# Performance work log

Hardware: AMD Instinct MI355X
Metric: run time of the kernel (lower is better)

The kernel has to match this reference:

```python
import jax, jax.numpy as jnp
import numpy as np

N = 100000      # nodes (dtype==2 subgraph)
E = 1600000     # edges
IN_DIM = 256
OUT_DIM = 64
FEAT_DIM = 64   # hard-coded by nn.Linear(64, out_dim) in dstfeat_fc


def setup_inputs() -> dict:
    key = jax.random.key(0)
    k1, k2, k3, k4, k5, k6 = jax.random.split(key, 6)
    h = jax.random.normal(k1, (N, IN_DIM), dtype=jnp.float32)
    feat = jax.random.normal(k2, (N, FEAT_DIM), dtype=jnp.float32)
    W_fc = jax.random.normal(k3, (OUT_DIM, IN_DIM), dtype=jnp.float32) * 0.05
    W_dst = jax.random.normal(k4, (OUT_DIM, FEAT_DIM), dtype=jnp.float32) * 0.05
    src = jax.random.randint(k5, (E,), 0, N, dtype=jnp.int64)
    dst = jax.random.randint(k6, (E,), 0, N, dtype=jnp.int64)
    return {"h": h, "feat": feat, "W_fc": W_fc, "W_dst": W_dst, "src": src, "dst": dst}


def reference(h, feat, W_fc, W_dst, src, dst):
    # node projections (done once per node, then gathered per edge)
    z = h @ W_fc.T            # [N, OUT]  (self.fc)
    df = feat @ W_dst.T       # [N, OUT]  (self.dstfeat_fc on dst 'feat')

    # per-edge attention logit: dot(z[src], dstfeat[dst])
    e = jnp.sum(z[src] * df[dst], axis=-1)          # [E]

    # segment softmax over incoming edges of each destination node
    emax = jax.ops.segment_max(e, dst, num_segments=N)
    emax = jnp.where(jnp.isfinite(emax), emax, 0.0)  # guard empty segments
    ex = jnp.exp(e - emax[dst])                      # [E]
    denom = jax.ops.segment_sum(ex, dst, num_segments=N)  # [N]

    # weighted neighbor aggregation: sum_e alpha_e * z[src_e] per dst
    num = jax.ops.segment_sum(ex[:, None] * z[src], dst, num_segments=N)  # [N, OUT]
    out = num / jnp.where(denom == 0, 1.0, denom)[:, None]
    return out
```

## Files before the change

### kernel.cpp

```cpp
#include <hip/hip_runtime.h>
#include <math.h>

typedef unsigned int uint32;
typedef __attribute__((ext_vector_type(8))) short bf16x8;
typedef __attribute__((ext_vector_type(4))) float f32x4;

__device__ __forceinline__ ushort f2bf(float f) {
  uint32 u = __builtin_bit_cast(uint32, f);
  uint32 r = (u + 0x7fff + ((u >> 16) & 1)) >> 16;
  return (ushort)r;
}
__device__ __forceinline__ float bf_lo(uint32 u) {
  return __builtin_bit_cast(float, u << 16);
}
__device__ __forceinline__ float bf_hi(uint32 u) {
  return __builtin_bit_cast(float, u & 0xffff0000u);
}

template <int K, bool BF16OUT>
__device__ __forceinline__ void gemm_body(const float* __restrict__ A,
                                          const float* __restrict__ W,
                                          ushort* __restrict__ Cb,
                                          float* __restrict__ C,
                                          int M, int bx, ushort* Ws) {
  const int t = threadIdx.x;
  const int lane = t & 63;
  const int w = t >> 6;
  const int quad = lane >> 4;
  const int l16 = lane & 15;
  const int rBase = bx * 128;
  const int WSTR = K + 8;

  const int kq4 = K >> 2;
  for (int idx = t; idx < 64 * kq4; idx += 256) {
    int row = idx / kq4, kq = idx - row * kq4;
    float4 v = *(const float4*)(W + (size_t)row * K + kq * 4);
    ushort4 b;
    b.x = f2bf(v.x); b.y = f2bf(v.y); b.z = f2bf(v.z); b.w = f2bf(v.w);
    *(ushort4*)&Ws[row * WSTR + kq * 4] = b;
  }
  __syncthreads();

  f32x4 acc[2][4];
  #pragma unroll
  for (int i = 0; i < 2; ++i)
    #pragma unroll
    for (int n = 0; n < 4; ++n) acc[i][n] = (f32x4){0.f, 0.f, 0.f, 0.f};

  const int r0 = min(rBase + w * 32 + l16, M - 1);
  const int r1 = min(rBase + w * 32 + 16 + l16, M - 1);
  const float* __restrict__ a0 = A + (size_t)r0 * K + quad * 8;
  const float* __restrict__ a1 = A + (size_t)r1 * K + quad * 8;

  #pragma unroll 2
  for (int kb = 0; kb < K; kb += 32) {
    float4 v00 = *(const float4*)(a0 + kb);
    float4 v01 = *(const float4*)(a0 + kb + 4);
    float4 v10 = *(const float4*)(a1 + kb);
    float4 v11 = *(const float4*)(a1 + kb + 4);
    bf16x8 af0, af1;
    af0[0] = (short)f2bf(v00.x); af0[1] = (short)f2bf(v00.y);
    af0[2] = (short)f2bf(v00.z); af0[3] = (short)f2bf(v00.w);
    af0[4] = (short)f2bf(v01.x); af0[5] = (short)f2bf(v01.y);
    af0[6] = (short)f2bf(v01.z); af0[7] = (short)f2bf(v01.w);
    af1[0] = (short)f2bf(v10.x); af1[1] = (short)f2bf(v10.y);
    af1[2] = (short)f2bf(v10.z); af1[3] = (short)f2bf(v10.w);
    af1[4] = (short)f2bf(v11.x); af1[5] = (short)f2bf(v11.y);
    af1[6] = (short)f2bf(v11.z); af1[7] = (short)f2bf(v11.w);

    bf16x8 bfrag[4];
    #pragma unroll
    for (int n = 0; n < 4; ++n)
      bfrag[n] = *(const bf16x8*)&Ws[(n * 16 + l16) * WSTR + kb + quad * 8];

    #pragma unroll
    for (int n = 0; n < 4; ++n) {
      acc[0][n] = __builtin_amdgcn_mfma_f32_16x16x32_bf16(af0, bfrag[n], acc[0][n], 0, 0, 0);
      acc[1][n] = __builtin_amdgcn_mfma_f32_16x16x32_bf16(af1, bfrag[n], acc[1][n], 0, 0, 0);
    }
  }

  #pragma unroll
  for (int i = 0; i < 2; ++i)
    #pragma unroll
    for (int nt = 0; nt < 4; ++nt)
      #pragma unroll
      for (int r = 0; r < 4; ++r) {
        int row = rBase + w * 32 + i * 16 + quad * 4 + r;
        int col = nt * 16 + l16;
        if (row < M) {
          if (BF16OUT)
            Cb[(size_t)row * 64 + col] = f2bf(acc[i][nt][r]);
          else
            C[(size_t)row * 64 + col] = acc[i][nt][r];
        }
      }
}

__global__ __launch_bounds__(256, 4) void gemm_both(const float* __restrict__ h,
                                                    const float* __restrict__ feat,
                                                    const float* __restrict__ W_fc,
                                                    const float* __restrict__ W_dst,
                                                    ushort* __restrict__ zb,
                                                    float* __restrict__ df,
                                                    int M, int gsplit) {
  __shared__ __align__(16) ushort Ws[64 * 264];
  if ((int)blockIdx.x < gsplit)
    gemm_body<256, true>(h, W_fc, zb, nullptr, M, (int)blockIdx.x, Ws);
  else
    gemm_body<64, false>(feat, W_dst, nullptr, df, M, (int)blockIdx.x - gsplit, Ws);
}

#define NBBITS 8
#define BKNODES 256
#define CH 4096
#define NBMAX 512

__global__ __launch_bounds__(256) void csr_count(const int* __restrict__ dst,
                                                 int* __restrict__ bCnt, int E, int NB) {
  __shared__ int lcnt[NBMAX];
  const int t = threadIdx.x;
  for (int i = t; i < NB; i += 256) lcnt[i] = 0;
  __syncthreads();
  const int c0 = blockIdx.x * CH, c1 = min(c0 + CH, E);
  for (int i = c0 + t; i < c1; i += 256) atomicAdd(&lcnt[dst[i] >> NBBITS], 1);
  __syncthreads();
  for (int b = t; b < NB; b += 256) {
    int c = lcnt[b];
    if (c) atomicAdd(&bCnt[b], c);
  }
}

__global__ __launch_bounds__(512) void csr_scan(const int* __restrict__ bCnt,
                                                int* __restrict__ bBase,
                                                int* __restrict__ bCursor,
                                                int* __restrict__ offsets,
                                                int NB, int N, int E) {
  __shared__ int wsum[8];
  const int t = threadIdx.x;
  const int lane = t & 63, wave = t >> 6;
  int x = (t < NB) ? bCnt[t] : 0;
  int inc = x;
  #pragma unroll
  for (int d = 1; d < 64; d <<= 1) {
    int o = __shfl_up(inc, d, 64);
    if (lane >= d) inc += o;
  }
  if (lane == 63) wsum[wave] = inc;
  __syncthreads();
  int wbase = 0;
  #pragma unroll
  for (int w = 0; w < 8; ++w)
    if (w < wave) wbase += wsum[w];
  int excl = wbase + inc - x;
  if (t < NB) {
    bBase[t] = excl;
    bCursor[t] = excl;
  }
  if (t == 0) {
    bBase[NB] = E;
    offsets[N] = E;
  }
}

__global__ __launch_bounds__(256) void csr_partition(const int* __restrict__ src,
                                                     const int* __restrict__ dst,
                                                     int* __restrict__ bCursor,
                                                     unsigned* __restrict__ packed,
                                                     int E, int NB) {
  __shared__ int lcnt[NBMAX];
  __shared__ int lbase[NBMAX];
  const int t = threadIdx.x;
  for (int i = t; i < NB; i += 256) lcnt[i] = 0;
  __syncthreads();
  const int c0 = blockIdx.x * CH, c1 = min(c0 + CH, E);
  for (int i = c0 + t; i < c1; i += 256) atomicAdd(&lcnt[dst[i] >> NBBITS], 1);
  __syncthreads();
  for (int b = t; b < NB; b += 256) {
    int c = lcnt[b];
    lbase[b] = c ? atomicAdd(&bCursor[b], c) : 0;
  }
  __syncthreads();
  for (int i = c0 + t; i < c1; i += 256) {
    int dv = dst[i];
    int b = dv >> NBBITS;
    int pos = atomicAdd(&lbase[b], 1);
    packed[pos] = ((unsigned)src[i] << NBBITS) | (unsigned)(dv & (BKNODES - 1));
  }
}

__global__ __launch_bounds__(256) void csr_finalize(const int* __restrict__ bBase,
                                                    const unsigned* __restrict__ packed,
                                                    int* __restrict__ edgeSrc,
                                                    int* __restrict__ offsets, int N) {
  __shared__ int sh[BKNODES];
  __shared__ int wsum[4];
  const int r = blockIdx.x;
  const int t = threadIdx.x;
  const int lane = t & 63, wave = t >> 6;
  const int base = bBase[r];
  const int endr = bBase[r + 1];
  sh[t] = 0;
  __syncthreads();
  for (int i = base + t; i < endr; i += 256)
    atomicAdd(&sh[packed[i] & (BKNODES - 1)], 1);
  __syncthreads();
  {
    int x = sh[t];
    int inc = x;
    #pragma unroll
    for (int d = 1; d < 64; d <<= 1) {
      int o = __shfl_up(inc, d, 64);
      if (lane >= d) inc += o;
    }
    if (lane == 63) wsum[wave] = inc;
    __syncthreads();
    int wbase = 0;
    #pragma unroll
    for (int w = 0; w < 4; ++w)
      if (w < wave) wbase += wsum[w];
    int excl = wbase + inc - x;
    __syncthreads();
    sh[t] = base + excl;
  }
  __syncthreads();
  const int node0 = r << NBBITS;
  {
    int g = node0 + t;
    if (g < N) offsets[g] = sh[t];
  }
  __syncthreads();
  for (int i = base + t; i < endr; i += 256) {
    unsigned v = packed[i];
    int pos = atomicAdd(&sh[v & (BKNODES - 1)], 1);
    edgeSrc[pos] = (int)(v >> NBBITS);
  }
}

__global__ __launch_bounds__(256) void aggregate(const ushort* __restrict__ zb,
                                                 const float* __restrict__ df,
                                                 const int* __restrict__ offsets,
                                                 const int* __restrict__ edgeSrc,
                                                 float* __restrict__ out, int N, int NW) {
  const int lane = threadIdx.x & 63;
  int d = __builtin_amdgcn_readfirstlane((int)((blockIdx.x * blockDim.x + threadIdx.x) >> 6));
  if (d >= N) return;
  const int g = lane >> 4;
  const int l16 = lane & 15;

  int beg = offsets[d];
  int end = offsets[d + 1];
  float4 df4 = *(const float4*)(df + (size_t)d * 64 + l16 * 4);

  while (true) {
    const int nd = d + NW;
    const int ndc = min(nd, N - 1);
    const int nbeg = offsets[ndc];
    const int nend = offsets[ndc + 1];
    const float4 ndf4 = *(const float4*)(df + (size_t)ndc * 64 + l16 * 4);

    float m = -INFINITY, l = 0.f;
    float ax = 0.f, ay = 0.f, az = 0.f, aw = 0.f;

    for (int j0 = beg; j0 < end; j0 += 32) {
      const int nst = min(8, (end - j0 + 3) >> 2);
      uint2 zf[8];
      float ew[8];
      float bm = -INFINITY;

      #pragma unroll
      for (int st = 0; st < 8; ++st) {
        if (st < nst) {
          const int eidx = j0 + st * 4 + g;
          const bool act = eidx < end;
          int s = 0;
          if (act) s = edgeSrc[eidx];
          zf[st] = *(const uint2*)(zb + (size_t)s * 64 + l16 * 4);
          float p = bf_lo(zf[st].x) * df4.x;
          p = fmaf(bf_hi(zf[st].x), df4.y, p);
          p = fmaf(bf_lo(zf[st].y), df4.z, p);
          p = fmaf(bf_hi(zf[st].y), df4.w, p);
          p += __shfl_xor(p, 1, 64);
          p += __shfl_xor(p, 2, 64);
          p += __shfl_xor(p, 4, 64);
          p += __shfl_xor(p, 8, 64);
          ew[st] = act ? p : -INFINITY;
          bm = fmaxf(bm, ew[st]);
        }
      }
      bm = fmaxf(bm, __shfl_xor(bm, 16, 64));
      bm = fmaxf(bm, __shfl_xor(bm, 32, 64));

      const float nm = fmaxf(m, bm);
      const float alpha = __expf(m - nm);
      float sw = 0.f;
      #pragma unroll
      for (int st = 0; st < 8; ++st) {
        if (st < nst) {
          const float w = __expf(ew[st] - nm);
          ew[st] = w;
          sw += w;
        }
      }
      sw += __shfl_xor(sw, 16, 64);
      sw += __shfl_xor(sw, 32, 64);
      l = l * alpha + sw;
      m = nm;

      ax *= alpha; ay *= alpha; az *= alpha; aw *= alpha;
      #pragma unroll
      for (int st = 0; st < 8; ++st) {
        if (st < nst) {
          const float w = ew[st];
          ax = fmaf(w, bf_lo(zf[st].x), ax);
          ay = fmaf(w, bf_hi(zf[st].x), ay);
          az = fmaf(w, bf_lo(zf[st].y), az);
          aw = fmaf(w, bf_hi(zf[st].y), aw);
        }
      }
    }

    ax += __shfl_xor(ax, 16, 64); ax += __shfl_xor(ax, 32, 64);
    ay += __shfl_xor(ay, 16, 64); ay += __shfl_xor(ay, 32, 64);
    az += __shfl_xor(az, 16, 64); az += __shfl_xor(az, 32, 64);
    aw += __shfl_xor(aw, 16, 64); aw += __shfl_xor(aw, 32, 64);

    if (lane < 16) {
      const float inv = (l > 0.f) ? (1.f / l) : 0.f;
      float4 o;
      o.x = ax * inv; o.y = ay * inv; o.z = az * inv; o.w = aw * inv;
      *(float4*)(out + (size_t)d * 64 + l16 * 4) = o;
    }

    if (nd >= N) break;
    d = nd; beg = nbeg; end = nend; df4 = ndf4;
  }
}

extern "C" void kernel_launch(void* const* d_in, const int* in_sizes, int n_in,
                              void* d_out, int out_size, void* d_ws, size_t ws_size,
                              hipStream_t stream) {
  const float* h     = (const float*)d_in[0];
  const float* feat  = (const float*)d_in[1];
  const float* W_fc  = (const float*)d_in[2];
  const float* W_dst = (const float*)d_in[3];
  const int*   src   = (const int*)d_in[4];
  const int*   dst   = (const int*)d_in[5];
  float* out = (float*)d_out;

  const int N = in_sizes[1] / 64;
  const int E = in_sizes[4];

  const int NB = (N + BKNODES - 1) >> NBBITS;
  const int nChunks = (E + CH - 1) / CH;

  char* ws = (char*)d_ws;
  ushort* zb = (ushort*)ws;
  float* df = (float*)(zb + (size_t)N * 64);
  int* offsets = (int*)(df + (size_t)N * 64);
  int* edgeSrc = offsets + N + 1;
  int* bCnt = edgeSrc + E;
  int* bBase = bCnt + NB;
  int* bCursor = bBase + NB + 1;
  unsigned* packed = (unsigned*)d_out;

  hipMemsetAsync(bCnt, 0, sizeof(int) * (size_t)NB, stream);

  const int gsplit = (N + 127) / 128;
  gemm_both<<<gsplit * 2, 256, 0, stream>>>(h, feat, W_fc, W_dst, zb, df, N, gsplit);

  csr_count<<<nChunks, 256, 0, stream>>>(dst, bCnt, E, NB);
  csr_scan<<<1, 512, 0, stream>>>(bCnt, bBase, bCursor, offsets, NB, N, E);
  csr_partition<<<nChunks, 256, 0, stream>>>(src, dst, bCursor, packed, E, NB);
  csr_finalize<<<NB, 256, 0, stream>>>(bBase, packed, edgeSrc, offsets, N);

  const int aggBlocks = 2048;
  const int NW = aggBlocks * 4;
  aggregate<<<aggBlocks, 256, 0, stream>>>(zb, df, offsets, edgeSrc, out, N, NW);
}
```

Before: 335.2 us.

## Fuse CSR count into GEMM launch, drop scan kernel, prefetch A tiles

Folds the edge-bucket counting into the GEMM kernel as extra blocks, so the counting runs alongside the projections in one launch. The separate single-block scan kernel is removed: partition and finalize each recompute the bucket prefix sum in shared memory, and partition takes its slots from a zeroed relative cursor array. The GEMM loop also register-prefetches the next A tile before converting the current one. This removes two launches and the serialization behind the one-block scan, in exchange for a redundant 512-entry scan in every partition and finalize block and more register pressure in the GEMM.

```diff
diff --git a/kernel.cpp b/kernel.cpp
--- a/kernel.cpp
+++ b/kernel.cpp
@@ -16,6 +16,11 @@
 __device__ __forceinline__ float bf_hi(uint32 u) {
   return __builtin_bit_cast(float, u & 0xffff0000u);
 }
+
+#define NBBITS 8
+#define BKNODES 256
+#define CH 4096
+#define NBMAX 512
 
 template <int K, bool BF16OUT>
 __device__ __forceinline__ void gemm_body(const float* __restrict__ A,
@@ -52,21 +57,31 @@
   const float* __restrict__ a0 = A + (size_t)r0 * K + quad * 8;
   const float* __restrict__ a1 = A + (size_t)r1 * K + quad * 8;
 
+  float4 c00 = *(const float4*)(a0);
+  float4 c01 = *(const float4*)(a0 + 4);
+  float4 c10 = *(const float4*)(a1);
+  float4 c11 = *(const float4*)(a1 + 4);
+
   #pragma unroll 2
   for (int kb = 0; kb < K; kb += 32) {
-    float4 v00 = *(const float4*)(a0 + kb);
-    float4 v01 = *(const float4*)(a0 + kb + 4);
-    float4 v10 = *(const float4*)(a1 + kb);
-    float4 v11 = *(const float4*)(a1 + kb + 4);
+    float4 n00, n01, n10, n11;
+    const bool more = (kb + 32 < K);
+    if (more) {
+      n00 = *(const float4*)(a0 + kb + 32);
+      n01 = *(const float4*)(a0 + kb + 36);
+      n10 = *(const float4*)(a1 + kb + 32);
+      n11 = *(const float4*)(a1 + kb + 36);
+    }
+
     bf16x8 af0, af1;
-    af0[0] = (short)f2bf(v00.x); af0[1] = (short)f2bf(v00.y);
-    af0[2] = (short)f2bf(v00.z); af0[3] = (short)f2bf(v00.w);
-    af0[4] = (short)f2bf(v01.x); af0[5] = (short)f2bf(v01.y);
-    af0[6] = (short)f2bf(v01.z); af0[7] = (short)f2bf(v01.w);
-    af1[0] = (short)f2bf(v10.x); af1[1] = (short)f2bf(v10.y);
-    af1[2] = (short)f2bf(v10.z); af1[3] = (short)f2bf(v10.w);
-    af1[4] = (short)f2bf(v11.x); af1[5] = (short)f2bf(v11.y);
-    af1[6] = (short)f2bf(v11.z); af1[7] = (short)f2bf(v11.w);
+    af0[0] = (short)f2bf(c00.x); af0[1] = (short)f2bf(c00.y);
+    af0[2] = (short)f2bf(c00.z); af0[3] = (short)f2bf(c00.w);
+    af0[4] = (short)f2bf(c01.x); af0[5] = (short)f2bf(c01.y);
+    af0[6] = (short)f2bf(c01.z); af0[7] = (short)f2bf(c01.w);
+    af1[0] = (short)f2bf(c10.x); af1[1] = (short)f2bf(c10.y);
+    af1[2] = (short)f2bf(c10.z); af1[3] = (short)f2bf(c10.w);
+    af1[4] = (short)f2bf(c11.x); af1[5] = (short)f2bf(c11.y);
+    af1[6] = (short)f2bf(c11.z); af1[7] = (short)f2bf(c11.w);
 
     bf16x8 bfrag[4];
     #pragma unroll
@@ -78,6 +93,8 @@
       acc[0][n] = __builtin_amdgcn_mfma_f32_16x16x32_bf16(af0, bfrag[n], acc[0][n], 0, 0, 0);
       acc[1][n] = __builtin_amdgcn_mfma_f32_16x16x32_bf16(af1, bfrag[n], acc[1][n], 0, 0, 0);
     }
+
+    if (more) { c00 = n00; c01 = n01; c10 = n10; c11 = n11; }
   }
 
   #pragma unroll
@@ -97,32 +114,13 @@
       }
 }
 
-__global__ __launch_bounds__(256, 4) void gemm_both(const float* __restrict__ h,
-                                                    const float* __restrict__ feat,
-                                                    const float* __restrict__ W_fc,
-                                                    const float* __restrict__ W_dst,
-                                                    ushort* __restrict__ zb,
-                                                    float* __restrict__ df,
-                                                    int M, int gsplit) {
-  __shared__ __align__(16) ushort Ws[64 * 264];
-  if ((int)blockIdx.x < gsplit)
-    gemm_body<256, true>(h, W_fc, zb, nullptr, M, (int)blockIdx.x, Ws);
-  else
-    gemm_body<64, false>(feat, W_dst, nullptr, df, M, (int)blockIdx.x - gsplit, Ws);
-}
-
-#define NBBITS 8
-#define BKNODES 256
-#define CH 4096
-#define NBMAX 512
-
-__global__ __launch_bounds__(256) void csr_count(const int* __restrict__ dst,
-                                                 int* __restrict__ bCnt, int E, int NB) {
-  __shared__ int lcnt[NBMAX];
+__device__ __forceinline__ void count_body(const int* __restrict__ dst,
+                                           int* __restrict__ bCnt,
+                                           int E, int NB, int cb, int* lcnt) {
   const int t = threadIdx.x;
   for (int i = t; i < NB; i += 256) lcnt[i] = 0;
   __syncthreads();
-  const int c0 = blockIdx.x * CH, c1 = min(c0 + CH, E);
+  const int c0 = cb * CH, c1 = min(c0 + CH, E);
   for (int i = c0 + t; i < c1; i += 256) atomicAdd(&lcnt[dst[i] >> NBBITS], 1);
   __syncthreads();
   for (int b = t; b < NB; b += 256) {
@@ -131,46 +129,59 @@
   }
 }
 
-__global__ __launch_bounds__(512) void csr_scan(const int* __restrict__ bCnt,
-                                                int* __restrict__ bBase,
-                                                int* __restrict__ bCursor,
-                                                int* __restrict__ offsets,
-                                                int NB, int N, int E) {
-  __shared__ int wsum[8];
-  const int t = threadIdx.x;
-  const int lane = t & 63, wave = t >> 6;
-  int x = (t < NB) ? bCnt[t] : 0;
-  int inc = x;
-  #pragma unroll
-  for (int d = 1; d < 64; d <<= 1) {
-    int o = __shfl_up(inc, d, 64);
-    if (lane >= d) inc += o;
-  }
-  if (lane == 63) wsum[wave] = inc;
-  __syncthreads();
-  int wbase = 0;
-  #pragma unroll
-  for (int w = 0; w < 8; ++w)
-    if (w < wave) wbase += wsum[w];
-  int excl = wbase + inc - x;
-  if (t < NB) {
-    bBase[t] = excl;
-    bCursor[t] = excl;
-  }
-  if (t == 0) {
-    bBase[NB] = E;
-    offsets[N] = E;
+__global__ __launch_bounds__(256, 4) void gemm_count(const float* __restrict__ h,
+                                                     const float* __restrict__ feat,
+                                                     const float* __restrict__ W_fc,
+                                                     const float* __restrict__ W_dst,
+                                                     ushort* __restrict__ zb,
+                                                     float* __restrict__ df,
+                                                     const int* __restrict__ dst,
+                                                     int* __restrict__ bCnt,
+                                                     int M, int gsplit, int E, int NB,
+                                                     int nChunks) {
+  __shared__ __align__(16) ushort Ws[64 * 264];
+  const int bx = (int)blockIdx.x;
+  if (bx < nChunks)
+    count_body(dst, bCnt, E, NB, bx, (int*)Ws);
+  else if (bx < nChunks + gsplit)
+    gemm_body<256, true>(h, W_fc, zb, nullptr, M, bx - nChunks, Ws);
+  else
+    gemm_body<64, false>(feat, W_dst, nullptr, df, M, bx - nChunks - gsplit, Ws);
+}
+
+__device__ __forceinline__ void block_scan512(const int* __restrict__ bCnt,
+                                              int NB, int* sc) {
+  const int t = threadIdx.x;
+  {
+    int v0 = (t < NB) ? bCnt[t] : 0;
+    int v1 = (t + 256 < NB) ? bCnt[t + 256] : 0;
+    sc[t] = v0;
+    sc[t + 256] = v1;
+  }
+  __syncthreads();
+  for (int off = 1; off < NBMAX; off <<= 1) {
+    int v0 = sc[t];
+    int a0 = (t >= off) ? sc[t - off] : 0;
+    int v1 = sc[t + 256];
+    int a1 = sc[t + 256 - off];
+    __syncthreads();
+    sc[t] = v0 + a0;
+    sc[t + 256] = v1 + a1;
+    __syncthreads();
   }
 }
 
 __global__ __launch_bounds__(256) void csr_partition(const int* __restrict__ src,
                                                      const int* __restrict__ dst,
-                                                     int* __restrict__ bCursor,
+                                                     const int* __restrict__ bCnt,
+                                                     int* __restrict__ relCur,
                                                      unsigned* __restrict__ packed,
                                                      int E, int NB) {
+  __shared__ int sc[NBMAX];
   __shared__ int lcnt[NBMAX];
   __shared__ int lbase[NBMAX];
   const int t = threadIdx.x;
+  block_scan512(bCnt, NB, sc);
   for (int i = t; i < NB; i += 256) lcnt[i] = 0;
   __syncthreads();
   const int c0 = blockIdx.x * CH, c1 = min(c0 + CH, E);
@@ -178,7 +189,7 @@
   __syncthreads();
   for (int b = t; b < NB; b += 256) {
     int c = lcnt[b];
-    lbase[b] = c ? atomicAdd(&bCursor[b], c) : 0;
+    lbase[b] = c ? (sc[b] - bCnt[b] + atomicAdd(&relCur[b], c)) : 0;
   }
   __syncthreads();
   for (int i = c0 + t; i < c1; i += 256) {
@@ -189,17 +200,21 @@
   }
 }
 
-__global__ __launch_bounds__(256) void csr_finalize(const int* __restrict__ bBase,
+__global__ __launch_bounds__(256) void csr_finalize(const int* __restrict__ bCnt,
                                                     const unsigned* __restrict__ packed,
                                                     int* __restrict__ edgeSrc,
-                                                    int* __restrict__ offsets, int N) {
+                                                    int* __restrict__ offsets,
+                                                    int N, int NB, int E) {
+  __shared__ int sc[NBMAX];
   __shared__ int sh[BKNODES];
   __shared__ int wsum[4];
   const int r = blockIdx.x;
   const int t = threadIdx.x;
   const int lane = t & 63, wave = t >> 6;
-  const int base = bBase[r];
-  const int endr = bBase[r + 1];
+  block_scan512(bCnt, NB, sc);
+  const int endr = sc[r];
+  const int base = endr - bCnt[r];
+  __syncthreads();
   sh[t] = 0;
   __syncthreads();
   for (int i = base + t; i < endr; i += 256)
@@ -229,6 +244,7 @@
     int g = node0 + t;
     if (g < N) offsets[g] = sh[t];
   }
+  if (r == NB - 1 && t == 0) offsets[N] = E;
   __syncthreads();
   for (int i = base + t; i < endr; i += 256) {
     unsigned v = packed[i];
@@ -360,19 +376,18 @@
   int* offsets = (int*)(df + (size_t)N * 64);
   int* edgeSrc = offsets + N + 1;
   int* bCnt = edgeSrc + E;
-  int* bBase = bCnt + NB;
-  int* bCursor = bBase + NB + 1;
+  int* relCur = bCnt + NB;
   unsigned* packed = (unsigned*)d_out;
 
-  hipMemsetAsync(bCnt, 0, sizeof(int) * (size_t)NB, stream);
+  hipMemsetAsync(bCnt, 0, sizeof(int) * (size_t)(2 * NB), stream);
 
   const int gsplit = (N + 127) / 128;
-  gemm_both<<<gsplit * 2, 256, 0, stream>>>(h, feat, W_fc, W_dst, zb, df, N, gsplit);
-
-  csr_count<<<nChunks, 256, 0, stream>>>(dst, bCnt, E, NB);
-  csr_scan<<<1, 512, 0, stream>>>(bCnt, bBase, bCursor, offsets, NB, N, E);
-  csr_partition<<<nChunks, 256, 0, stream>>>(src, dst, bCursor, packed, E, NB);
-  csr_finalize<<<NB, 256, 0, stream>>>(bBase, packed, edgeSrc, offsets, N);
+  gemm_count<<<nChunks + gsplit * 2, 256, 0, stream>>>(h, feat, W_fc, W_dst, zb, df,
+                                                       dst, bCnt, N, gsplit, E, NB,
+                                                       nChunks);
+
+  csr_partition<<<nChunks, 256, 0, stream>>>(src, dst, bCnt, relCur, packed, E, NB);
+  csr_finalize<<<NB, 256, 0, stream>>>(bCnt, packed, edgeSrc, offsets, N, NB, E);
 
   const int aggBlocks = 2048;
   const int NW = aggBlocks * 4;
```

After: 328.7 us. Within noise of the previous version (-1.9%).
